# Kernel tuning notes

Measured on AMD Instinct MI355X. Metric: run time of the kernel, lower is better.

## Reference

```python
import jax, jax.numpy as jnp
import numpy as np

B, CIN, CMID, H, W = 2, 64, 128, 96, 96
KWIN = 7          # attention_window
DIL = 1           # attention_stride (dilation)
GROUPS = 16
EPS = 1e-5
SCALE = float(np.sqrt(CMID))  # torch: math.sqrt(intermediate_channels), multiplies logits (NATTEN semantics)


def group_norm(x, w, b):
    # x: [B,C,H,W], 16 groups, per-channel affine
    Bx, C, Hx, Wx = x.shape
    xg = x.reshape(Bx, GROUPS, C // GROUPS, Hx, Wx)
    mu = xg.mean(axis=(2, 3, 4), keepdims=True)
    var = xg.var(axis=(2, 3, 4), keepdims=True)
    xg = (xg - mu) * jax.lax.rsqrt(var + EPS)
    return xg.reshape(Bx, C, Hx, Wx) * w[None, :, None, None] + b[None, :, None, None]


def neighborhood_attention_2d(q, k, v, ksz, scale):
    # q,k,v: [B,H,W,C]; NATTEN-style neighborhood attention, dilation=1.
    Hh, Ww = q.shape[1], q.shape[2]
    half = ksz // 2
    # window start per query, clipped so every query sees exactly ksz keys per axis
    si = jnp.clip(jnp.arange(Hh) - half, 0, Hh - ksz)          # [H]
    sj = jnp.clip(jnp.arange(Ww) - half, 0, Ww - ksz)          # [W]
    idx_i = si[:, None] + jnp.arange(ksz)[None, :]             # [H,k]
    idx_j = sj[:, None] + jnp.arange(ksz)[None, :]             # [W,k]
    kw = k[:, idx_i][:, :, :, idx_j]                           # [B,H,k,W,k,C]
    vw = v[:, idx_i][:, :, :, idx_j]                           # [B,H,k,W,k,C]
    logits = jnp.einsum('bijc,biajkc->bijak', q, kw) * scale   # [B,H,W,k,k]
    Bq = logits.shape[0]
    attn = jax.nn.softmax(logits.reshape(Bq, Hh, Ww, ksz * ksz), axis=-1)
    attn = attn.reshape(Bq, Hh, Ww, ksz, ksz)
    return jnp.einsum('bijak,biajkc->bijc', attn, vw)          # [B,H,W,C]


def setup_inputs() -> dict:
    key = jax.random.key(0)
    ks = jax.random.split(key, 6)

    def wtz(k, shape, fan):
        return (jax.random.normal(k, shape, jnp.float32) / np.sqrt(fan)).astype(jnp.float32)

    return {
        'x': jax.random.normal(ks[0], (B, CIN, H, W), jnp.float32),
        'gn_w': jnp.ones((CIN,), jnp.float32),
        'gn_b': jnp.zeros((CIN,), jnp.float32),
        'conv_w': wtz(ks[1], (CMID, CIN, 3, 3), CIN * 9),
        'conv_b': jnp.zeros((CMID,), jnp.float32),
        'q_w': wtz(ks[2], (CMID, CMID), CMID),
        'q_b': jnp.zeros((CMID,), jnp.float32),
        'k_w': wtz(ks[3], (CMID, CMID), CMID),
        'k_b': jnp.zeros((CMID,), jnp.float32),
        'v_w': wtz(ks[4], (CMID, CMID), CMID),
        'v_b': jnp.zeros((CMID,), jnp.float32),
    }


def reference(x, gn_w, gn_b, conv_w, conv_b, q_w, q_b, k_w, k_b, v_w, v_b):
    xn = group_norm(x, gn_w, gn_b)
    # 3x3 conv, padding=1 + exact GELU (torch nn.GELU default)
    f = jax.lax.conv_general_dilated(
        xn, conv_w, window_strides=(1, 1), padding=((1, 1), (1, 1)),
        dimension_numbers=('NCHW', 'OIHW', 'NCHW')) + conv_b[None, :, None, None]
    f = jax.nn.gelu(f, approximate=False)
    # 1x1 QKV convs
    q = jnp.einsum('bchw,oc->bohw', f, q_w) + q_b[None, :, None, None]
    k = jnp.einsum('bchw,oc->bohw', f, k_w) + k_b[None, :, None, None]
    v = jnp.einsum('bchw,oc->bohw', f, v_w) + v_b[None, :, None, None]
    # to NHWC (singleton head dim squeezed)
    qh = q.transpose(0, 2, 3, 1)
    kh = k.transpose(0, 2, 3, 1)
    vh = v.transpose(0, 2, 3, 1)
    ksz = min(KWIN, f.shape[2], f.shape[3])
    ksz -= 1 if ksz % 2 == 0 else 0
    out = neighborhood_attention_2d(qh, kh, vh, ksz, SCALE)
    return out.transpose(0, 3, 1, 2)  # back to NCHW
```

## Files before the change

kernel.cpp:

```cpp
#include <hip/hip_runtime.h>
#include <math.h>

#define Hh 96
#define Ww 96
#define HW 9216
#define CIN 64
#define CMID 128
#define NAT_SCALE 11.313708498984761f

typedef __attribute__((ext_vector_type(4))) float f32x4;
typedef __attribute__((ext_vector_type(8))) short short8;

__device__ __forceinline__ unsigned short f2bf(float x) {
    union { float f; unsigned u; } v; v.f = x;
    unsigned r = v.u + 0x7FFF + ((v.u >> 16) & 1);
    return (unsigned short)(r >> 16);
}
__device__ __forceinline__ float bf2f(unsigned short h) {
    union { unsigned u; float f; } v; v.u = (unsigned)h << 16;
    return v.f;
}

__global__ __launch_bounds__(256) void prep_kernel(const float* __restrict__ x,
    float2* __restrict__ partials,
    const float* __restrict__ cw, const float* __restrict__ qw,
    const float* __restrict__ kw_, const float* __restrict__ vw,
    unsigned short* __restrict__ wch, unsigned short* __restrict__ wcl,
    unsigned short* __restrict__ wqh, unsigned short* __restrict__ wql,
    unsigned short* __restrict__ xh, unsigned short* __restrict__ xl)
{
    int bid = blockIdx.x, tid = threadIdx.x;
    if (bid < 512) {
        size_t base = (size_t)(bid >> 4) * 36864 + (size_t)(bid & 15) * 2304;
        float s = 0.f, s2 = 0.f;
        #pragma unroll
        for (int i = 0; i < 9; ++i) {
            float v = x[base + i * 256 + tid];
            s += v; s2 += v * v;
        }
        #pragma unroll
        for (int d = 1; d < 64; d <<= 1) {
            s  += __shfl_xor(s, d);
            s2 += __shfl_xor(s2, d);
        }
        __shared__ float as[4], as2[4];
        int wid = tid >> 6, lane = tid & 63;
        if (lane == 0) { as[wid] = s; as2[wid] = s2; }
        __syncthreads();
        if (tid == 0) {
            float2 r = { as[0]+as[1]+as[2]+as[3], as2[0]+as2[1]+as2[2]+as2[3] };
            partials[bid] = r;
        }
    } else if (bid < 992) {
        int t = (bid - 512) * 256 + tid;
        if (t < 73728) {
            int e = t & 7, l = (t >> 3) & 63, fr = (t >> 9) & 1;
            int ocg = (t >> 10) & 3, s2 = t >> 12;
            int s = s2 >> 1, ch = s2 & 1;
            int oc = ocg * 32 + fr * 16 + (l & 15);
            int c  = ch * 32 + (l >> 4) * 8 + e;
            float v = cw[oc * 576 + c * 9 + s];
            unsigned short hi = f2bf(v);
            wch[t] = hi; wcl[t] = f2bf(v - bf2f(hi));
        } else {
            int t2 = t - 73728;
            int e = t2 & 7, l = (t2 >> 3) & 63, fr = (t2 >> 9) & 1;
            int ocg = (t2 >> 10) & 3, kc2 = (t2 >> 12) & 3, m = t2 >> 14;
            int oc = ocg * 32 + fr * 16 + (l & 15);
            int c  = kc2 * 32 + (l >> 4) * 8 + e;
            const float* W = (m == 0) ? qw : (m == 1) ? kw_ : vw;
            float v = W[oc * 128 + c];
            unsigned short hi = f2bf(v);
            wqh[t2] = hi; wql[t2] = f2bf(v - bf2f(hi));
        }
    } else {
        int t = (bid - 992) * 256 + tid;
        if (t < 6208) {
            int b = t / 3104, r = t - b * 3104;
            int pos = r >> 3, gc = r & 7;
            int y, xx;
            if (pos < 98)      { y = 0;          xx = pos; }
            else if (pos < 196){ y = 97;         xx = pos - 98; }
            else if (pos < 292){ y = pos - 195;  xx = 0; }
            else               { y = pos - 291;  xx = 97; }
            size_t off = ((size_t)(b * 98 + y) * 98 + xx) * 64 + gc * 8;
            short8 z = {0,0,0,0,0,0,0,0};
            *(short8*)(xh + off) = z;
            *(short8*)(xl + off) = z;
        }
    }
}

__global__ __launch_bounds__(256) void gnapply_kernel(const float* __restrict__ x,
    const float2* __restrict__ partials,
    const float* __restrict__ gw, const float* __restrict__ gb,
    unsigned short* __restrict__ xh, unsigned short* __restrict__ xl)
{
    __shared__ float tin[64 * 25];
    __shared__ float sgld[32];
    int blk = blockIdx.x;
    int b = blk / 384, r1 = blk - b * 384;
    int y = r1 >> 2, q = r1 & 3;
    int tid = threadIdx.x;

    {
        float2 pv = partials[b * 256 + tid];
        float s = pv.x, s2 = pv.y;
        #pragma unroll
        for (int d = 1; d < 16; d <<= 1) {
            s  += __shfl_xor(s, d);
            s2 += __shfl_xor(s2, d);
        }
        if ((tid & 15) == 0) {
            const float invN = 1.f / 36864.f;
            float mean = s * invN;
            float var  = s2 * invN - mean * mean;
            sgld[(tid >> 4) * 2]     = mean;
            sgld[(tid >> 4) * 2 + 1] = rsqrtf(var + 1e-5f);
        }
    }
    #pragma unroll
    for (int i = 0; i < 6; ++i) {
        int idx = i * 256 + tid;
        int c = idx / 24, xx = idx - c * 24;
        tin[c * 25 + xx] = x[((size_t)(b * CIN + c)) * HW + y * Ww + q * 24 + xx];
    }
    __syncthreads();
    #pragma unroll
    for (int i = 0; i < 6; ++i) {
        int idx = i * 256 + tid;
        int xx = idx >> 6, c = idx & 63;
        float v = tin[c * 25 + xx];
        float val = (v - sgld[(c >> 2) * 2]) * sgld[(c >> 2) * 2 + 1] * gw[c] + gb[c];
        unsigned short hi = f2bf(val);
        unsigned short lo = f2bf(val - bf2f(hi));
        size_t dst = ((size_t)(b * 98 + y + 1) * 98 + q * 24 + xx + 1) * 64 + c;
        xh[dst] = hi; xl[dst] = lo;
    }
}

#define MFMA3(ACC, AH, AL, BH, BL) \
    ACC = __builtin_amdgcn_mfma_f32_16x16x32_bf16(AL, BH, ACC, 0, 0, 0); \
    ACC = __builtin_amdgcn_mfma_f32_16x16x32_bf16(AH, BL, ACC, 0, 0, 0); \
    ACC = __builtin_amdgcn_mfma_f32_16x16x32_bf16(AH, BH, ACC, 0, 0, 0);

__global__ __launch_bounds__(256) void convqkv_kernel(
    const unsigned short* __restrict__ xh, const unsigned short* __restrict__ xl,
    const unsigned short* __restrict__ wch, const unsigned short* __restrict__ wcl,
    const float* __restrict__ cb,
    const unsigned short* __restrict__ wqh, const unsigned short* __restrict__ wql,
    const float* __restrict__ qbias, const float* __restrict__ kbias,
    const float* __restrict__ vbias,
    float* __restrict__ qo, float* __restrict__ ko, float* __restrict__ vo)
{
    __shared__ __align__(16) short ph_s[3840];
    __shared__ __align__(16) short pl_s[3840];
    __shared__ __align__(16) short fh_s[4096];
    __shared__ __align__(16) short fl_s[4096];
    int bid = blockIdx.x;
    int swz = (bid & 7) * 72 + (bid >> 3);
    int b = swz / 288, rem = swz - b * 288;
    int ty = rem / 12, tx = rem - ty * 12;
    int y0 = ty * 4, x0 = tx * 8;
    int tid = threadIdx.x;

    for (int g = tid; g < 480; g += 256) {
        int row = g / 80, r2 = g - row * 80;
        int col = r2 >> 3, gc = r2 & 7;
        size_t srcoff = ((size_t)(b * 98 + y0 + row) * 98 + x0 + col) * 64 + gc * 8;
        int dst = ((row * 10 + col) << 6) + ((gc ^ (col & 7)) << 3);
        *(short8*)&ph_s[dst] = *(const short8*)(xh + srcoff);
        *(short8*)&pl_s[dst] = *(const short8*)(xl + srcoff);
    }
    __syncthreads();

    int ocg = tid >> 6, l = tid & 63;
    int l15 = l & 15, l4 = l >> 4;
    int oc0 = ocg * 32;
    int p0 = l15, p1 = 16 + l15;
    int r0 = p0 >> 3, xc = p0 & 7;

    f32x4 c00 = {0.f,0.f,0.f,0.f}, c01 = {0.f,0.f,0.f,0.f};
    f32x4 c10 = {0.f,0.f,0.f,0.f}, c11 = {0.f,0.f,0.f,0.f};

    #pragma unroll 3
    for (int s = 0; s < 9; ++s) {
        int dy = s / 3, dx = s - dy * 3;
        int colA = xc + dx, cswz = (colA & 7) << 3;
        #pragma unroll
        for (int ch = 0; ch < 2; ++ch) {
            int gr = (ch * 4 + l4) << 3;
            int ai0 = (((r0 + dy) * 10 + colA) << 6) + (gr ^ cswz);
            int ai1 = (((r0 + 2 + dy) * 10 + colA) << 6) + (gr ^ cswz);
            short8 a0h = *(const short8*)&ph_s[ai0];
            short8 a0l = *(const short8*)&pl_s[ai0];
            short8 a1h = *(const short8*)&ph_s[ai1];
            short8 a1l = *(const short8*)&pl_s[ai1];
            int s2 = s * 2 + ch;
            int wb = ((s2 * 4 + ocg) * 2) * 512 + l * 8;
            short8 b0h = *(const short8*)(wch + wb);
            short8 b0l = *(const short8*)(wcl + wb);
            short8 b1h = *(const short8*)(wch + wb + 512);
            short8 b1l = *(const short8*)(wcl + wb + 512);
            MFMA3(c00, a0h, a0l, b0h, b0l)
            MFMA3(c01, a0h, a0l, b1h, b1l)
            MFMA3(c10, a1h, a1l, b0h, b0l)
            MFMA3(c11, a1h, a1l, b1h, b1l)
        }
    }

    float bias0 = cb[oc0 + l15], bias1 = cb[oc0 + 16 + l15];
    #pragma unroll
    for (int mf = 0; mf < 2; ++mf) {
        #pragma unroll
        for (int nf = 0; nf < 2; ++nf) {
            f32x4 a = (mf == 0) ? (nf == 0 ? c00 : c01) : (nf == 0 ? c10 : c11);
            float bs = nf == 0 ? bias0 : bias1;
            int oc = oc0 + nf * 16 + l15;
            #pragma unroll
            for (int rr = 0; rr < 4; ++rr) {
                int p = mf * 16 + l4 * 4 + rr;
                float v = a[rr] + bs;
                float g = 0.5f * v * (1.f + erff(v * 0.70710678118654752f));
                unsigned short hi = f2bf(g);
                unsigned short lo = f2bf(g - bf2f(hi));
                int di = p * 128 + ((((oc >> 3) ^ (p & 7)) << 3) | (oc & 7));
                fh_s[di] = (short)hi;
                fl_s[di] = (short)lo;
            }
        }
    }
    __syncthreads();

    int sw0 = (p0 & 7) << 3, sw1 = (p1 & 7) << 3;
    #pragma unroll 1
    for (int m = 0; m < 3; ++m) {
        const float* Bi = (m == 0) ? qbias : (m == 1) ? kbias : vbias;
        float* Om = (m == 0) ? qo : (m == 1) ? ko : vo;
        f32x4 d00 = {0.f,0.f,0.f,0.f}, d01 = {0.f,0.f,0.f,0.f};
        f32x4 d10 = {0.f,0.f,0.f,0.f}, d11 = {0.f,0.f,0.f,0.f};
        #pragma unroll
        for (int kc2 = 0; kc2 < 4; ++kc2) {
            int gr2 = (kc2 * 4 + l4) << 3;
            int i0 = p0 * 128 + (gr2 ^ sw0);
            int i1 = p1 * 128 + (gr2 ^ sw1);
            short8 ah0 = *(const short8*)&fh_s[i0];
            short8 al0 = *(const short8*)&fl_s[i0];
            short8 ah1 = *(const short8*)&fh_s[i1];
            short8 al1 = *(const short8*)&fl_s[i1];
            int wb = (((m * 4 + kc2) * 4 + ocg) * 2) * 512 + l * 8;
            short8 b0h = *(const short8*)(wqh + wb);
            short8 b0l = *(const short8*)(wql + wb);
            short8 b1h = *(const short8*)(wqh + wb + 512);
            short8 b1l = *(const short8*)(wql + wb + 512);
            MFMA3(d00, ah0, al0, b0h, b0l)
            MFMA3(d01, ah0, al0, b1h, b1l)
            MFMA3(d10, ah1, al1, b0h, b0l)
            MFMA3(d11, ah1, al1, b1h, b1l)
        }
        float bm0 = Bi[oc0 + l15], bm1 = Bi[oc0 + 16 + l15];
        #pragma unroll
        for (int mf = 0; mf < 2; ++mf) {
            #pragma unroll
            for (int nf = 0; nf < 2; ++nf) {
                f32x4 a = (mf == 0) ? (nf == 0 ? d00 : d01) : (nf == 0 ? d10 : d11);
                float bs = nf == 0 ? bm0 : bm1;
                int oc = oc0 + nf * 16 + l15;
                #pragma unroll
                for (int rr = 0; rr < 4; ++rr) {
                    int p = mf * 16 + l4 * 4 + rr;
                    int yy = y0 + (p >> 3), xx = x0 + (p & 7);
                    Om[((size_t)(b * HW + yy * Ww + xx)) * CMID + oc] = a[rr] + bs;
                }
            }
        }
    }
}

__global__ __launch_bounds__(256) void nat_kernel(const float* __restrict__ q,
    const float* __restrict__ k, const float* __restrict__ v,
    float* __restrict__ out)
{
    __shared__ __align__(16) float Kl[12800];
    int bid = blockIdx.x;
    int swz = (bid & 7) * 144 + (bid >> 3);
    int b = swz / 576, rem = swz - b * 576;
    int ti = rem / 24, tj = rem - ti * 24;
    int i0 = ti * 4, j0 = tj * 4;
    int ui = i0 - 3; ui = ui < 0 ? 0 : (ui > 86 ? 86 : ui);
    int uj = j0 - 3; uj = uj < 0 ? 0 : (uj > 86 ? 86 : uj);
    int tid = threadIdx.x;

    const float4* ksrc = (const float4*)k;
    float4* Kl4 = (float4*)Kl;
    #pragma unroll
    for (int it = 0; it < 13; ++it) {
        int idx = it * 256 + tid;
        if (idx < 3200) {
            int row = idx >> 5, c4 = idx & 31;
            int ur = row / 10, uc = row - ur * 10;
            size_t gp = ((size_t)(b * HW + (ui + ur) * Ww + (uj + uc))) * 32 + c4;
            Kl4[row * 32 + (c4 ^ (row & 7))] = ksrc[gp];
        }
    }
    __syncthreads();

    int wid = tid >> 6, lane = tid & 63;
    int gy = wid >> 1, gx = wid & 1;
    int iq0 = i0 + 2 * gy, jq0 = j0 + 2 * gx;

    int si0 = iq0 - 3; si0 = si0 < 0 ? 0 : (si0 > 89 ? 89 : si0);
    int si1 = iq0 - 2; si1 = si1 < 0 ? 0 : (si1 > 89 ? 89 : si1);
    int sj0 = jq0 - 3; sj0 = sj0 < 0 ? 0 : (sj0 > 89 ? 89 : sj0);
    int sj1 = jq0 - 2; sj1 = sj1 < 0 ? 0 : (sj1 > 89 ? 89 : sj1);
    int gsi = si0 > 88 ? 88 : si0;
    int gsj = sj0 > 88 ? 88 : sj0;
    int oi0 = si0 - gsi, oi1 = si1 - gsi, oj0 = sj0 - gsj, oj1 = sj1 - gsj;
    int goi = gsi - ui, goj = gsj - uj;

    int wr = lane >> 3, wc = lane & 7;
    int R = (goi + wr) * 10 + (goj + wc);
    int Rs = R * 32, Rx = R & 7;

    const float4* qp0 = (const float4*)(q + (size_t)(b * HW + iq0 * Ww + jq0) * CMID);
    float a0 = 0.f, a1 = 0.f, a2 = 0.f, a3 = 0.f;
    #pragma unroll 8
    for (int c = 0; c < 32; ++c) {
        float4 kv = Kl4[Rs + (c ^ Rx)];
        float4 q0 = qp0[c], q1 = qp0[c + 32], q2 = qp0[c + 3072], q3 = qp0[c + 3104];
        a0 = fmaf(q0.x, kv.x, a0); a0 = fmaf(q0.y, kv.y, a0);
        a0 = fmaf(q0.z, kv.z, a0); a0 = fmaf(q0.w, kv.w, a0);
        a1 = fmaf(q1.x, kv.x, a1); a1 = fmaf(q1.y, kv.y, a1);
        a1 = fmaf(q1.z, kv.z, a1); a1 = fmaf(q1.w, kv.w, a1);
        a2 = fmaf(q2.x, kv.x, a2); a2 = fmaf(q2.y, kv.y, a2);
        a2 = fmaf(q2.z, kv.z, a2); a2 = fmaf(q2.w, kv.w, a2);
        a3 = fmaf(q3.x, kv.x, a3); a3 = fmaf(q3.y, kv.y, a3);
        a3 = fmaf(q3.z, kv.z, a3); a3 = fmaf(q3.w, kv.w, a3);
    }

    float l0 = ((unsigned)(wr - oi0) <= 6u && (unsigned)(wc - oj0) <= 6u) ? a0 * NAT_SCALE : -INFINITY;
    float l1 = ((unsigned)(wr - oi0) <= 6u && (unsigned)(wc - oj1) <= 6u) ? a1 * NAT_SCALE : -INFINITY;
    float l2 = ((unsigned)(wr - oi1) <= 6u && (unsigned)(wc - oj0) <= 6u) ? a2 * NAT_SCALE : -INFINITY;
    float l3 = ((unsigned)(wr - oi1) <= 6u && (unsigned)(wc - oj1) <= 6u) ? a3 * NAT_SCALE : -INFINITY;
    float m0 = l0, m1 = l1, m2 = l2, m3 = l3;
    #pragma unroll
    for (int d = 1; d < 64; d <<= 1) {
        m0 = fmaxf(m0, __shfl_xor(m0, d)); m1 = fmaxf(m1, __shfl_xor(m1, d));
        m2 = fmaxf(m2, __shfl_xor(m2, d)); m3 = fmaxf(m3, __shfl_xor(m3, d));
    }
    float e0 = __expf(l0 - m0), e1 = __expf(l1 - m1);
    float e2 = __expf(l2 - m2), e3 = __expf(l3 - m3);
    float s0 = e0, s1 = e1, s2 = e2, s3 = e3;
    #pragma unroll
    for (int d = 1; d < 64; d <<= 1) {
        s0 += __shfl_xor(s0, d); s1 += __shfl_xor(s1, d);
        s2 += __shfl_xor(s2, d); s3 += __shfl_xor(s3, d);
    }
    float w0 = e0 / s0, w1 = e1 / s1, w2 = e2 / s2, w3 = e3 / s3;

    int base2 = b * HW + gsi * Ww + gsj;
    const float2* vbase = (const float2*)(v + (size_t)base2 * CMID);
    float2 o0 = {0.f, 0.f}, o1 = {0.f, 0.f}, o2 = {0.f, 0.f}, o3 = {0.f, 0.f};
    #pragma unroll
    for (int w = 0; w < 64; ++w) {
        int off = ((w >> 3) * Ww + (w & 7)) * 64;
        float2 vv = vbase[off + lane];
        float b0 = __shfl(w0, w), b1 = __shfl(w1, w);
        float b2 = __shfl(w2, w), b3 = __shfl(w3, w);
        o0.x = fmaf(b0, vv.x, o0.x); o0.y = fmaf(b0, vv.y, o0.y);
        o1.x = fmaf(b1, vv.x, o1.x); o1.y = fmaf(b1, vv.y, o1.y);
        o2.x = fmaf(b2, vv.x, o2.x); o2.y = fmaf(b2, vv.y, o2.y);
        o3.x = fmaf(b3, vv.x, o3.x); o3.y = fmaf(b3, vv.y, o3.y);
    }

    size_t ob = ((size_t)(b * CMID + 2 * lane)) * HW + iq0 * Ww + jq0;
    float2 r0 = {o0.x, o1.x}, r1 = {o0.y, o1.y};
    float2 r2 = {o2.x, o3.x}, r3 = {o2.y, o3.y};
    *(float2*)(out + ob)           = r0;
    *(float2*)(out + ob + HW)      = r1;
    *(float2*)(out + ob + Ww)      = r2;
    *(float2*)(out + ob + HW + Ww) = r3;
}

extern "C" void kernel_launch(void* const* d_in, const int* in_sizes, int n_in,
                              void* d_out, int out_size, void* d_ws, size_t ws_size,
                              hipStream_t stream) {
    const float* x      = (const float*)d_in[0];
    const float* gn_w   = (const float*)d_in[1];
    const float* gn_b   = (const float*)d_in[2];
    const float* conv_w = (const float*)d_in[3];
    const float* conv_b = (const float*)d_in[4];
    const float* q_w    = (const float*)d_in[5];
    const float* q_b    = (const float*)d_in[6];
    const float* k_w    = (const float*)d_in[7];
    const float* k_b    = (const float*)d_in[8];
    const float* v_w    = (const float*)d_in[9];
    const float* v_b    = (const float*)d_in[10];

    const size_t XNP = (size_t)2 * 98 * 98 * 64;
    float* ws    = (float*)d_ws;
    float2* partials = (float2*)ws;
    float* qb_   = ws + 1024;
    float* kb_   = qb_ + (size_t)2 * CMID * HW;
    float* vb_   = kb_ + (size_t)2 * CMID * HW;
    unsigned short* xnh = (unsigned short*)(vb_ + (size_t)2 * CMID * HW);
    unsigned short* xnl = xnh + XNP;
    unsigned short* wch = xnl + XNP;
    unsigned short* wcl = wch + 73728;
    unsigned short* wqh = wcl + 73728;
    unsigned short* wql = wqh + 49152;

    prep_kernel<<<1017, 256, 0, stream>>>(x, partials, conv_w, q_w, k_w, v_w,
                                          wch, wcl, wqh, wql, xnh, xnl);
    gnapply_kernel<<<768, 256, 0, stream>>>(x, partials, gn_w, gn_b, xnh, xnl);
    convqkv_kernel<<<576, 256, 0, stream>>>(xnh, xnl, wch, wcl, conv_b,
                                            wqh, wql, q_b, k_b, v_b,
                                            qb_, kb_, vb_);
    nat_kernel<<<1152, 256, 0, stream>>>(qb_, kb_, vb_, (float*)d_out);
}
```

Baseline: 75.81 us.

## Fuse GroupNorm apply and padding into conv tile load, drop gnapply kernel

```diff
diff --git a/kernel.cpp b/kernel.cpp
--- a/kernel.cpp
+++ b/kernel.cpp
@@ -26,8 +26,7 @@
     const float* __restrict__ cw, const float* __restrict__ qw,
     const float* __restrict__ kw_, const float* __restrict__ vw,
     unsigned short* __restrict__ wch, unsigned short* __restrict__ wcl,
-    unsigned short* __restrict__ wqh, unsigned short* __restrict__ wql,
-    unsigned short* __restrict__ xh, unsigned short* __restrict__ xl)
+    unsigned short* __restrict__ wqh, unsigned short* __restrict__ wql)
 {
     int bid = blockIdx.x, tid = threadIdx.x;
     if (bid < 512) {
@@ -51,7 +50,7 @@
             float2 r = { as[0]+as[1]+as[2]+as[3], as2[0]+as2[1]+as2[2]+as2[3] };
             partials[bid] = r;
         }
-    } else if (bid < 992) {
+    } else {
         int t = (bid - 512) * 256 + tid;
         if (t < 73728) {
             int e = t & 7, l = (t >> 3) & 63, fr = (t >> 9) & 1;
@@ -73,69 +72,6 @@
             unsigned short hi = f2bf(v);
             wqh[t2] = hi; wql[t2] = f2bf(v - bf2f(hi));
         }
-    } else {
-        int t = (bid - 992) * 256 + tid;
-        if (t < 6208) {
-            int b = t / 3104, r = t - b * 3104;
-            int pos = r >> 3, gc = r & 7;
-            int y, xx;
-            if (pos < 98)      { y = 0;          xx = pos; }
-            else if (pos < 196){ y = 97;         xx = pos - 98; }
-            else if (pos < 292){ y = pos - 195;  xx = 0; }
-            else               { y = pos - 291;  xx = 97; }
-            size_t off = ((size_t)(b * 98 + y) * 98 + xx) * 64 + gc * 8;
-            short8 z = {0,0,0,0,0,0,0,0};
-            *(short8*)(xh + off) = z;
-            *(short8*)(xl + off) = z;
-        }
-    }
-}
-
-__global__ __launch_bounds__(256) void gnapply_kernel(const float* __restrict__ x,
-    const float2* __restrict__ partials,
-    const float* __restrict__ gw, const float* __restrict__ gb,
-    unsigned short* __restrict__ xh, unsigned short* __restrict__ xl)
-{
-    __shared__ float tin[64 * 25];
-    __shared__ float sgld[32];
-    int blk = blockIdx.x;
-    int b = blk / 384, r1 = blk - b * 384;
-    int y = r1 >> 2, q = r1 & 3;
-    int tid = threadIdx.x;
-
-    {
-        float2 pv = partials[b * 256 + tid];
-        float s = pv.x, s2 = pv.y;
-        #pragma unroll
-        for (int d = 1; d < 16; d <<= 1) {
-            s  += __shfl_xor(s, d);
-            s2 += __shfl_xor(s2, d);
-        }
-        if ((tid & 15) == 0) {
-            const float invN = 1.f / 36864.f;
-            float mean = s * invN;
-            float var  = s2 * invN - mean * mean;
-            sgld[(tid >> 4) * 2]     = mean;
-            sgld[(tid >> 4) * 2 + 1] = rsqrtf(var + 1e-5f);
-        }
-    }
-    #pragma unroll
-    for (int i = 0; i < 6; ++i) {
-        int idx = i * 256 + tid;
-        int c = idx / 24, xx = idx - c * 24;
-        tin[c * 25 + xx] = x[((size_t)(b * CIN + c)) * HW + y * Ww + q * 24 + xx];
-    }
-    __syncthreads();
-    #pragma unroll
-    for (int i = 0; i < 6; ++i) {
-        int idx = i * 256 + tid;
-        int xx = idx >> 6, c = idx & 63;
-        float v = tin[c * 25 + xx];
-        float val = (v - sgld[(c >> 2) * 2]) * sgld[(c >> 2) * 2 + 1] * gw[c] + gb[c];
-        unsigned short hi = f2bf(val);
-        unsigned short lo = f2bf(val - bf2f(hi));
-        size_t dst = ((size_t)(b * 98 + y + 1) * 98 + q * 24 + xx + 1) * 64 + c;
-        xh[dst] = hi; xl[dst] = lo;
     }
 }
 
@@ -145,7 +81,8 @@
     ACC = __builtin_amdgcn_mfma_f32_16x16x32_bf16(AH, BH, ACC, 0, 0, 0);
 
 __global__ __launch_bounds__(256) void convqkv_kernel(
-    const unsigned short* __restrict__ xh, const unsigned short* __restrict__ xl,
+    const float* __restrict__ x, const float2* __restrict__ partials,
+    const float* __restrict__ gw, const float* __restrict__ gb,
     const unsigned short* __restrict__ wch, const unsigned short* __restrict__ wcl,
     const float* __restrict__ cb,
     const unsigned short* __restrict__ wqh, const unsigned short* __restrict__ wql,
@@ -157,6 +94,7 @@
     __shared__ __align__(16) short pl_s[3840];
     __shared__ __align__(16) short fh_s[4096];
     __shared__ __align__(16) short fl_s[4096];
+    __shared__ float sgld[32];
     int bid = blockIdx.x;
     int swz = (bid & 7) * 72 + (bid >> 3);
     int b = swz / 288, rem = swz - b * 288;
@@ -164,13 +102,51 @@
     int y0 = ty * 4, x0 = tx * 8;
     int tid = threadIdx.x;
 
-    for (int g = tid; g < 480; g += 256) {
-        int row = g / 80, r2 = g - row * 80;
-        int col = r2 >> 3, gc = r2 & 7;
-        size_t srcoff = ((size_t)(b * 98 + y0 + row) * 98 + x0 + col) * 64 + gc * 8;
-        int dst = ((row * 10 + col) << 6) + ((gc ^ (col & 7)) << 3);
-        *(short8*)&ph_s[dst] = *(const short8*)(xh + srcoff);
-        *(short8*)&pl_s[dst] = *(const short8*)(xl + srcoff);
+    float raw[15];
+    #pragma unroll
+    for (int it = 0; it < 15; ++it) {
+        int idx = it * 256 + tid;
+        int c = idx / 60, p = idx - c * 60;
+        int row = p / 10, col = p - row * 10;
+        int gy = y0 - 1 + row, gx = x0 - 1 + col;
+        float v = 0.f;
+        if ((unsigned)gy < 96u && (unsigned)gx < 96u)
+            v = x[((size_t)(b * CIN + c)) * HW + gy * Ww + gx];
+        raw[it] = v;
+    }
+
+    {
+        float2 pv = partials[b * 256 + tid];
+        float s = pv.x, s2 = pv.y;
+        #pragma unroll
+        for (int d = 1; d < 16; d <<= 1) {
+            s  += __shfl_xor(s, d);
+            s2 += __shfl_xor(s2, d);
+        }
+        if ((tid & 15) == 0) {
+            const float invN = 1.f / 36864.f;
+            float mean = s * invN;
+            float var  = s2 * invN - mean * mean;
+            sgld[(tid >> 4) * 2]     = mean;
+            sgld[(tid >> 4) * 2 + 1] = rsqrtf(var + 1e-5f);
+        }
+    }
+    __syncthreads();
+
+    #pragma unroll
+    for (int it = 0; it < 15; ++it) {
+        int idx = it * 256 + tid;
+        int c = idx / 60, p = idx - c * 60;
+        int row = p / 10, col = p - row * 10;
+        int gy = y0 - 1 + row, gx = x0 - 1 + col;
+        bool ok = ((unsigned)gy < 96u && (unsigned)gx < 96u);
+        float val = ok ? ((raw[it] - sgld[(c >> 2) * 2]) * sgld[(c >> 2) * 2 + 1]
+                          * gw[c] + gb[c]) : 0.f;
+        unsigned short hi = f2bf(val);
+        unsigned short lo = f2bf(val - bf2f(hi));
+        int di = ((row * 10 + col) << 6) + ((((c >> 3) ^ (col & 7)) << 3) | (c & 7));
+        ph_s[di] = (short)hi;
+        pl_s[di] = (short)lo;
     }
     __syncthreads();
 
@@ -397,23 +373,20 @@
     const float* v_w    = (const float*)d_in[9];
     const float* v_b    = (const float*)d_in[10];
 
-    const size_t XNP = (size_t)2 * 98 * 98 * 64;
     float* ws    = (float*)d_ws;
     float2* partials = (float2*)ws;
     float* qb_   = ws + 1024;
     float* kb_   = qb_ + (size_t)2 * CMID * HW;
     float* vb_   = kb_ + (size_t)2 * CMID * HW;
-    unsigned short* xnh = (unsigned short*)(vb_ + (size_t)2 * CMID * HW);
-    unsigned short* xnl = xnh + XNP;
-    unsigned short* wch = xnl + XNP;
+    unsigned short* wch = (unsigned short*)(vb_ + (size_t)2 * CMID * HW);
     unsigned short* wcl = wch + 73728;
     unsigned short* wqh = wcl + 73728;
     unsigned short* wql = wqh + 49152;
 
-    prep_kernel<<<1017, 256, 0, stream>>>(x, partials, conv_w, q_w, k_w, v_w,
-                                          wch, wcl, wqh, wql, xnh, xnl);
-    gnapply_kernel<<<768, 256, 0, stream>>>(x, partials, gn_w, gn_b, xnh, xnl);
-    convqkv_kernel<<<576, 256, 0, stream>>>(xnh, xnl, wch, wcl, conv_b,
+    prep_kernel<<<992, 256, 0, stream>>>(x, partials, conv_w, q_w, k_w, v_w,
+                                         wch, wcl, wqh, wql);
+    convqkv_kernel<<<576, 256, 0, stream>>>(x, partials, gn_w, gn_b,
+                                            wch, wcl, conv_b,
                                             wqh, wql, q_b, k_b, v_b,
                                             qb_, kb_, vb_);
     nat_kernel<<<1152, 256, 0, stream>>>(qb_, kb_, vb_, (float*)d_out);
```

New measurement: 74.97 us. Within noise of the previous version (-1.1%).
